# Kernel optimization log

Hardware: AMD Instinct MI355X
Metric: run time of the kernel (lower is better)

## Reference

```python
import jax, jax.numpy as jnp
import numpy as np

N_NODES = 200_000
N_EDGES = 6_400_000
EMB = 32      # emb_hidden_dim
HID = 16      # hidden_dim
BY = 4        # num_birthyear_disc
NSYMP = 15    # num_symp (rm_feature=-999)
NOPT = 3      # replace_missing_value='replace'


def setup_inputs() -> dict:
    key = jax.random.key(0)
    ks = jax.random.split(key, 12)
    # node features: [one-hot birth (4) | gender (1) | 15 symptom codes]
    birth_cat = jax.random.randint(ks[0], (N_NODES,), 0, BY)
    birth_oh = jax.nn.one_hot(birth_cat, BY, dtype=jnp.int32)
    gender = jax.random.randint(ks[1], (N_NODES, 1), 0, 2, dtype=jnp.int32)
    symp = jax.random.randint(ks[2], (N_NODES, NSYMP), 0, NOPT, dtype=jnp.int32)
    x = jnp.concatenate([birth_oh, gender, symp], axis=1)  # [N, 20] int32
    edge_index = jax.random.randint(ks[3], (2, N_EDGES), 0, N_NODES, dtype=jnp.int64)
    s = 0.1
    return {
        "x": x,
        "edge_index": edge_index,
        "birth_table": jax.random.normal(ks[4], (BY, EMB), jnp.float32) * s,
        "gender_table": jax.random.normal(ks[5], (2, EMB), jnp.float32) * s,
        "symp_tables": jax.random.normal(ks[6], (NSYMP, NOPT, EMB), jnp.float32) * s,
        "W1": jax.random.normal(ks[7], (EMB, HID), jnp.float32) * s,
        "b1": jnp.zeros((HID,), jnp.float32),
        "W2": jax.random.normal(ks[8], (HID, HID), jnp.float32) * s,
        "b2": jnp.zeros((HID,), jnp.float32),
        "Wl": jax.random.normal(ks[9], (HID, 1), jnp.float32) * s,
        "bl": jnp.zeros((1,), jnp.float32),
    }


def _gcn_conv(h, W, b, src, tgt, n):
    # PyG GCNConv: linear (no bias) -> symmetric normalization w/ self-loops -> scatter-add -> +bias
    h = h @ W                                    # [N, out]
    msg = h[src] * None if False else h[src]     # gather source features
    deg = jax.ops.segment_sum(jnp.ones_like(tgt, dtype=h.dtype), tgt, num_segments=n)
    dinv = jnp.where(deg > 0, jax.lax.rsqrt(jnp.maximum(deg, 1e-12)), 0.0)
    norm = dinv[src] * dinv[tgt]                 # [E+N]
    out = jax.ops.segment_sum(norm[:, None] * msg, tgt, num_segments=n)
    return out + b


def reference(x, edge_index, birth_table, gender_table, symp_tables, W1, b1, W2, b2, Wl, bl):
    n = x.shape[0]
    birth_idx = jnp.argmax(x[:, :BY], axis=1)                 # column of the 1 in one-hot
    birth_embs = birth_table[birth_idx]                       # [N, EMB]
    gender_embs = gender_table[x[:, BY].astype(jnp.int32)]    # [N, EMB]
    symp_idx = x[:, -NSYMP:].astype(jnp.int32)                # [N, 15]
    feat_embs = jnp.mean(symp_tables[jnp.arange(NSYMP)[None, :], symp_idx], axis=1)  # [N, EMB]
    h = (birth_embs + gender_embs + feat_embs) / 3.0          # mean of the three stacks
    # dropout is identity in eval mode
    # self-loops added once (identical for both convs)
    loop = jnp.arange(n, dtype=edge_index.dtype)
    src = jnp.concatenate([edge_index[0], loop])
    tgt = jnp.concatenate([edge_index[1], loop])
    h = jax.nn.elu(_gcn_conv(h, W1, b1, src, tgt, n))
    h = _gcn_conv(h, W2, b2, src, tgt, n)
    return h @ Wl + bl                                        # [N, 1]
```

## Files before the change

kernel.cpp:

```cpp
#include <hip/hip_runtime.h>
#include <hip/hip_fp16.h>
#include <math.h>

#define EMB 32
#define HID 16
#define BY 4
#define NSYMP 15
#define NOPT 3
#define XCOLS (BY + 1 + NSYMP)

#define BSHIFT 8
#define BSZ 256
#define EPB 4096
#define NBCAP 1024
#define SPT 4
#define LSTCAP 10240

#define SCAN_T 256
#define SCAN_E 32
#define SCAN_B (SCAN_T * SCAN_E)

__device__ __forceinline__ unsigned int wave_incl_scan(unsigned int v, int lane) {
#pragma unroll
    for (int off = 1; off < 64; off <<= 1) {
        unsigned int u = __shfl_up(v, off, 64);
        if (lane >= off) v += u;
    }
    return v;
}

__global__ __launch_bounds__(256) void k_hist(const int* __restrict__ tgt,
                                              unsigned int* __restrict__ H,
                                              int nE, int gb1, int nbins) {
    __shared__ unsigned int h[NBCAP];
    int b = blockIdx.x, tid = threadIdx.x;
    for (int k = tid; k < NBCAP; k += 256) h[k] = 0;
    __syncthreads();
    int e0 = b * EPB;
    int ecnt = min(EPB, nE - e0);
    for (int k = tid; k < ecnt; k += 256)
        atomicAdd(&h[(unsigned)tgt[e0 + k] >> BSHIFT], 1u);
    __syncthreads();
    for (int q = tid; q < nbins; q += 256) H[(size_t)q * gb1 + b] = h[q];
}

__global__ __launch_bounds__(256) void k_bsum(const unsigned int* __restrict__ A,
                                              unsigned int* __restrict__ bsum, int m) {
    __shared__ unsigned int s[SCAN_T];
    int base = blockIdx.x * SCAN_B + threadIdx.x * SCAN_E;
    unsigned int t = 0;
#pragma unroll
    for (int k = 0; k < SCAN_E; ++k) { int idx = base + k; if (idx < m) t += A[idx]; }
    s[threadIdx.x] = t; __syncthreads();
    for (int off = SCAN_T / 2; off > 0; off >>= 1) {
        if (threadIdx.x < off) s[threadIdx.x] += s[threadIdx.x + off];
        __syncthreads();
    }
    if (threadIdx.x == 0) bsum[blockIdx.x] = s[0];
}

__global__ __launch_bounds__(512) void k_bscan(const unsigned int* __restrict__ bsum,
                                               unsigned int* __restrict__ boff, int nb) {
    __shared__ unsigned int s[512];
    unsigned int v = (threadIdx.x < (unsigned)nb) ? bsum[threadIdx.x] : 0u;
    s[threadIdx.x] = v; __syncthreads();
    for (int off = 1; off < 512; off <<= 1) {
        unsigned int t = (threadIdx.x >= (unsigned)off) ? s[threadIdx.x - off] : 0u;
        __syncthreads();
        s[threadIdx.x] += t;
        __syncthreads();
    }
    if (threadIdx.x < (unsigned)nb) boff[threadIdx.x] = s[threadIdx.x] - v;
}

__global__ __launch_bounds__(256) void k_scan2(const unsigned int* __restrict__ A,
                                               const unsigned int* __restrict__ boff,
                                               unsigned int* __restrict__ S, int m, int total) {
    __shared__ unsigned int s[SCAN_T];
    int tid = threadIdx.x;
    int base = blockIdx.x * SCAN_B + tid * SCAN_E;
    unsigned int t = 0;
#pragma unroll
    for (int k = 0; k < SCAN_E; ++k) { int idx = base + k; if (idx < m) t += A[idx]; }
    s[tid] = t; __syncthreads();
    unsigned int own = t;
    for (int off = 1; off < SCAN_T; off <<= 1) {
        unsigned int u = (tid >= off) ? s[tid - off] : 0u;
        __syncthreads();
        s[tid] += u;
        __syncthreads();
    }
    unsigned int run = boff[blockIdx.x] + s[tid] - own;
#pragma unroll
    for (int k = 0; k < SCAN_E; ++k) {
        int idx = base + k;
        if (idx < m) { S[idx] = run; run += A[idx]; }
    }
    if (blockIdx.x == 0 && tid == 0) S[m] = (unsigned int)total;
}

__global__ __launch_bounds__(256) void k_scat(const int* __restrict__ tgt,
                                              const int* __restrict__ src,
                                              const unsigned int* __restrict__ S,
                                              int* __restrict__ bp,
                                              int nE, int gb1, int nbins) {
    __shared__ int bpv[EPB];
    __shared__ unsigned short qid[EPB];
    __shared__ unsigned int cur[NBCAP];
    __shared__ unsigned int dif[NBCAP];
    __shared__ unsigned int wsum[4];
    int b = blockIdx.x, tid = threadIdx.x;
    int lane = tid & 63, wid = tid >> 6;
    for (int k = tid; k < NBCAP; k += 256) cur[k] = 0;
    __syncthreads();
    int e0 = b * EPB;
    int ecnt = min(EPB, nE - e0);

    for (int k = tid; k < ecnt; k += 256)
        atomicAdd(&cur[(unsigned)tgt[e0 + k] >> BSHIFT], 1u);
    __syncthreads();

    unsigned int lv[SPT]; unsigned int tsum = 0;
#pragma unroll
    for (int k = 0; k < SPT; ++k) {
        int f = SPT * tid + k;
        lv[k] = tsum; tsum += cur[f];
    }
    unsigned int incl = wave_incl_scan(tsum, lane);
    if (lane == 63) wsum[wid] = incl;
    __syncthreads();
    unsigned int woff = 0;
    for (int w = 0; w < wid; ++w) woff += wsum[w];
    unsigned int excl = woff + incl - tsum;
    __syncthreads();
#pragma unroll
    for (int k = 0; k < SPT; ++k) {
        int f = SPT * tid + k;
        cur[f] = excl + lv[k]; dif[f] = excl + lv[k];
    }
    __syncthreads();
    for (int q = tid; q < nbins; q += 256)
        dif[q] = S[(size_t)q * gb1 + b] - dif[q];
    __syncthreads();

    for (int k = tid; k < ecnt; k += 256) {
        int t = tgt[e0 + k];
        int q = (unsigned)t >> BSHIFT;
        unsigned int lpos = atomicAdd(&cur[q], 1u);
        bpv[lpos] = (src[e0 + k] << BSHIFT) | (t & (BSZ - 1));
        qid[lpos] = (unsigned short)q;
    }
    __syncthreads();

    for (int k = tid; k < ecnt; k += 256) {
        int q = qid[k];
        bp[dif[q] + k] = bpv[k];
    }
}

__global__ __launch_bounds__(256) void k_bcsr(const unsigned int* __restrict__ S,
                                              const int* __restrict__ bp,
                                              unsigned int* __restrict__ rowptr,
                                              int* __restrict__ col,
                                              float* __restrict__ dinv,
                                              int n, int gb1) {
    __shared__ int lst[LSTCAP];
    __shared__ unsigned int h[BSZ];
    __shared__ unsigned int cu[BSZ];
    __shared__ unsigned int wsum[4];
    int q = blockIdx.x, tid = threadIdx.x;
    int lane = tid & 63, wid = tid >> 6;
    h[tid] = 0;
    __syncthreads();
    unsigned int e0 = S[(size_t)q * gb1];
    unsigned int e1 = S[(size_t)(q + 1) * gb1];
    int cnt = (int)(e1 - e0);
    for (int k = tid; k < cnt; k += 256)
        atomicAdd(&h[bp[e0 + k] & (BSZ - 1)], 1u);
    __syncthreads();
    unsigned int own = h[tid];
    unsigned int incl = wave_incl_scan(own, lane);
    if (lane == 63) wsum[wid] = incl;
    __syncthreads();
    unsigned int woff = 0;
    for (int w = 0; w < wid; ++w) woff += wsum[w];
    unsigned int excl = woff + incl - own;
    cu[tid] = excl;
    int i = (q << BSHIFT) + tid;
    if (i <= n) rowptr[i] = e0 + excl;
    if (i < n) {
        float d = (float)(own + 1u);
        float r = rsqrtf(d);
        r = r * (1.5f - 0.5f * d * r * r);
        dinv[i] = r;
    }
    __syncthreads();
    for (int k = tid; k < cnt; k += 256) {
        int v = bp[e0 + k];
        unsigned int pos = atomicAdd(&cu[v & (BSZ - 1)], 1u);
        lst[pos] = (unsigned)v >> BSHIFT;
    }
    __syncthreads();
    for (int k = tid; k < cnt; k += 256)
        col[e0 + k] = lst[k];
}

__global__ __launch_bounds__(256) void k_embed(const int* __restrict__ x,
                                               const float* __restrict__ birth_t,
                                               const float* __restrict__ gender_t,
                                               const float* __restrict__ symp_t,
                                               const float* __restrict__ W1,
                                               const float* __restrict__ dinv,
                                               __half* __restrict__ A16, int n) {
    __shared__ float sB[BY * EMB];
    __shared__ float sG[2 * EMB];
    __shared__ float sS[NSYMP * NOPT * EMB];
    __shared__ float sW[EMB * HID];
    for (int k = threadIdx.x; k < BY * EMB; k += blockDim.x) sB[k] = birth_t[k];
    for (int k = threadIdx.x; k < 2 * EMB; k += blockDim.x) sG[k] = gender_t[k];
    for (int k = threadIdx.x; k < NSYMP * NOPT * EMB; k += blockDim.x) sS[k] = symp_t[k];
    for (int k = threadIdx.x; k < EMB * HID; k += blockDim.x) sW[k] = W1[k];
    __syncthreads();

    int i = blockIdx.x * blockDim.x + threadIdx.x;
    if (i >= n) return;

    const int* xr = x + (size_t)i * XCOLS;
    int xv[XCOLS];
#pragma unroll
    for (int k = 0; k < XCOLS; ++k) xv[k] = xr[k];

    int bi = 0;
#pragma unroll
    for (int k = 1; k < BY; ++k) if (xv[k] > xv[bi]) bi = k;
    int gi = xv[BY];

    float ssum[EMB];
#pragma unroll
    for (int k = 0; k < EMB; ++k) ssum[k] = 0.f;
#pragma unroll
    for (int j = 0; j < NSYMP; ++j) {
        const float* row = &sS[(j * NOPT + xv[BY + 1 + j]) * EMB];
#pragma unroll
        for (int k = 0; k < EMB; ++k) ssum[k] += row[k];
    }

    float h[EMB];
#pragma unroll
    for (int k = 0; k < EMB; ++k)
        h[k] = (sB[bi * EMB + k] + sG[gi * EMB + k] + ssum[k] * (1.f / 15.f)) * (1.f / 3.f);

    float hp[HID];
#pragma unroll
    for (int j = 0; j < HID; ++j) hp[j] = 0.f;
#pragma unroll
    for (int k = 0; k < EMB; ++k) {
        float hv = h[k];
#pragma unroll
        for (int j = 0; j < HID; ++j) hp[j] += hv * sW[k * HID + j];
    }

    float dv = dinv[i];
    __half2 t2[8];
#pragma unroll
    for (int j = 0; j < 8; ++j)
        t2[j] = __floats2half2_rn(dv * hp[2 * j], dv * hp[2 * j + 1]);
    uint4* o = (uint4*)(A16 + (size_t)i * HID);
    o[0] = *(uint4*)&t2[0];
    o[1] = *(uint4*)&t2[4];
}

__global__ __launch_bounds__(256) void k_gmid5(const unsigned int* __restrict__ rowptr,
                                               const int* __restrict__ col,
                                               const __half* __restrict__ A16,
                                               const float* __restrict__ dinv,
                                               const float* __restrict__ W2,
                                               const float* __restrict__ b1,
                                               const float* __restrict__ Wl,
                                               float* __restrict__ z, int n) {
    __shared__ float sW[HID * HID];
    __shared__ float sb[HID];
    __shared__ float sw[HID];
    __shared__ float sAcc[16][HID];
    if (threadIdx.x < HID * HID) sW[threadIdx.x] = W2[threadIdx.x];
    if (threadIdx.x < HID) { sb[threadIdx.x] = b1[threadIdx.x]; sw[threadIdx.x] = Wl[threadIdx.x]; }
    __syncthreads();

    int gg = threadIdx.x >> 4;
    int l  = threadIdx.x & 15;
    int p  = l >> 1;
    int hc = l & 1;
    int i = blockIdx.x * 16 + gg;
    bool valid = (i < n);

    unsigned int r0 = 0, r1 = 0;
    if (valid) { r0 = rowptr[i]; r1 = rowptr[i + 1]; }

    float a[8];
#pragma unroll
    for (int k = 0; k < 8; ++k) a[k] = 0.f;

    unsigned int e = r0;
    for (; e + 16 <= r1; e += 16) {
        int s0 = col[e + p];
        int s1 = col[e + 8 + p];
        uint4 raw0 = *((const uint4*)(A16 + (size_t)s0 * HID) + hc);
        uint4 raw1 = *((const uint4*)(A16 + (size_t)s1 * HID) + hc);
        const __half2* h0 = (const __half2*)&raw0;
        const __half2* h1 = (const __half2*)&raw1;
#pragma unroll
        for (int k = 0; k < 4; ++k) {
            float2 f0 = __half22float2(h0[k]);
            float2 f1 = __half22float2(h1[k]);
            a[2 * k]     += f0.x + f1.x;
            a[2 * k + 1] += f0.y + f1.y;
        }
    }
    for (; e + 8 <= r1; e += 8) {
        int s0 = col[e + p];
        uint4 raw0 = *((const uint4*)(A16 + (size_t)s0 * HID) + hc);
        const __half2* h0 = (const __half2*)&raw0;
#pragma unroll
        for (int k = 0; k < 4; ++k) {
            float2 f0 = __half22float2(h0[k]);
            a[2 * k]     += f0.x;
            a[2 * k + 1] += f0.y;
        }
    }
    if (e + p < r1) {
        int s0 = col[e + p];
        uint4 raw0 = *((const uint4*)(A16 + (size_t)s0 * HID) + hc);
        const __half2* h0 = (const __half2*)&raw0;
#pragma unroll
        for (int k = 0; k < 4; ++k) {
            float2 f0 = __half22float2(h0[k]);
            a[2 * k]     += f0.x;
            a[2 * k + 1] += f0.y;
        }
    }
#pragma unroll
    for (int k = 0; k < 8; ++k) {
        a[k] += __shfl_xor(a[k], 2, 64);
        a[k] += __shfl_xor(a[k], 4, 64);
        a[k] += __shfl_xor(a[k], 8, 64);
    }
    if (l < 2) {
        float4* d0 = (float4*)&sAcc[gg][hc * 8];
        d0[0] = make_float4(a[0], a[1], a[2], a[3]);
        d0[1] = make_float4(a[4], a[5], a[6], a[7]);
    }
    __syncthreads();

    float dv = valid ? dinv[i] : 0.f;
    float self = valid ? __half2float(A16[(size_t)i * HID + l]) : 0.f;
    float v = dv * (sAcc[gg][l] + self) + sb[l];
    float h1 = (v > 0.f) ? v : expm1f(v);

    int lanebase = (threadIdx.x & 63) & ~15;
    float hp = 0.f;
#pragma unroll
    for (int k = 0; k < HID; ++k)
        hp += __shfl(h1, lanebase + k, 64) * sW[k * HID + l];
    float pz = dv * hp * sw[l];
#pragma unroll
    for (int off = 8; off > 0; off >>= 1) pz += __shfl_xor(pz, off, 64);
    if (l == 0 && valid) z[i] = pz;
}

__global__ __launch_bounds__(256) void k_gfin4(const unsigned int* __restrict__ rowptr,
                                               const int* __restrict__ col,
                                               const float* __restrict__ z,
                                               const float* __restrict__ dinv,
                                               const float* __restrict__ b2,
                                               const float* __restrict__ Wl,
                                               const float* __restrict__ bl,
                                               float* __restrict__ out, int n) {
    __shared__ float sc0;
    if (threadIdx.x == 0) {
        float c = 0.f;
#pragma unroll
        for (int k = 0; k < HID; ++k) c += b2[k] * Wl[k];
        sc0 = c + bl[0];
    }
    __syncthreads();

    int i = blockIdx.x * blockDim.x + threadIdx.x;
    if (i >= n) return;

    unsigned int r0 = rowptr[i];
    unsigned int r1 = rowptr[i + 1];
    float s0 = 0.f, s1 = 0.f, s2 = 0.f, s3 = 0.f;
    float s4 = 0.f, s5 = 0.f, s6 = 0.f, s7 = 0.f;
    unsigned int e = r0;
    for (; e + 8 <= r1; e += 8) {
        s0 += z[col[e + 0]]; s1 += z[col[e + 1]];
        s2 += z[col[e + 2]]; s3 += z[col[e + 3]];
        s4 += z[col[e + 4]]; s5 += z[col[e + 5]];
        s6 += z[col[e + 6]]; s7 += z[col[e + 7]];
    }
    for (; e < r1; ++e) s0 += z[col[e]];
    float s = ((s0 + s1) + (s2 + s3)) + ((s4 + s5) + (s6 + s7));
    out[i] = dinv[i] * (s + z[i]) + sc0;
}

extern "C" void kernel_launch(void* const* d_in, const int* in_sizes, int n_in,
                              void* d_out, int out_size, void* d_ws, size_t ws_size,
                              hipStream_t stream) {
    const int*   x        = (const int*)d_in[0];
    const int*   ei       = (const int*)d_in[1];
    const float* birth_t  = (const float*)d_in[2];
    const float* gender_t = (const float*)d_in[3];
    const float* symp_t   = (const float*)d_in[4];
    const float* W1       = (const float*)d_in[5];
    const float* b1       = (const float*)d_in[6];
    const float* W2       = (const float*)d_in[7];
    const float* b2       = (const float*)d_in[8];
    const float* Wl       = (const float*)d_in[9];
    const float* bl       = (const float*)d_in[10];
    float*       out      = (float*)d_out;

    const int n  = in_sizes[0] / XCOLS;
    const int nE = in_sizes[1] / 2;
    const int* src = ei;
    const int* tgt = ei + nE;

    const int nbuck = (n + BSZ - 1) >> BSHIFT;
    const int gb1   = (nE + EPB - 1) / EPB;
    const int M     = nbuck * gb1;
    const int nb    = (M + SCAN_B - 1) / SCAN_B;

    char* ws = (char*)d_ws;
    size_t off = 0;
    auto alloc = [&](size_t bytes) { char* p = ws + off; off = (off + bytes + 255) & ~(size_t)255; return p; };
    unsigned int* H      = (unsigned int*)alloc((size_t)M * 4);
    unsigned int* S      = (unsigned int*)alloc(((size_t)M + 1) * 4);
    unsigned int* bsum   = (unsigned int*)alloc(512 * 4);
    unsigned int* boff   = (unsigned int*)alloc(512 * 4);
    int*          bp     = (int*)alloc((size_t)nE * 4);
    int*          col    = (int*)alloc((size_t)nE * 4);
    unsigned int* rowptr = (unsigned int*)alloc(((size_t)n + 1) * 4);
    float*        dinv   = (float*)alloc((size_t)n * 4);
    __half*       A16    = (__half*)alloc((size_t)n * HID * 2);
    float*        z      = (float*)alloc((size_t)n * 4);

    const int BLK = 256;
    const int gN    = (n + BLK - 1) / BLK;
    const int gNode = (n + 15) / 16;

    k_hist <<<gb1, BLK, 0, stream>>>(tgt, H, nE, gb1, nbuck);
    k_bsum <<<nb, SCAN_T, 0, stream>>>(H, bsum, M);
    k_bscan<<<1, 512, 0, stream>>>(bsum, boff, nb);
    k_scan2<<<nb, SCAN_T, 0, stream>>>(H, boff, S, M, nE);
    k_scat <<<gb1, BLK, 0, stream>>>(tgt, src, S, bp, nE, gb1, nbuck);
    k_bcsr <<<nbuck, BLK, 0, stream>>>(S, bp, rowptr, col, dinv, n, gb1);
    k_embed<<<gN, BLK, 0, stream>>>(x, birth_t, gender_t, symp_t, W1, dinv, A16, n);
    k_gmid5<<<gNode, BLK, 0, stream>>>(rowptr, col, A16, dinv, W2, b1, Wl, z, n);
    k_gfin4<<<gN, BLK, 0, stream>>>(rowptr, col, z, dinv, b2, Wl, bl, out, n);
}
```

Before: 258.9 us.

## Use fixed 512 blocks for bucket scatter and write edges directly to global

The edge histogram and scatter now run on a fixed grid of 512 blocks with about 12.5k edges each, down from 1563 blocks of 4096 edges. That shrinks the histogram and scan matrix. The scatter kernel no longer re-counts, scans and stages edges in shared memory; it seeds per-bucket cursors from the global scan and writes each packed edge straight to its global slot through a shared atomic. This removes a shared-memory pass and several barriers, but the global writes become scattered, and fewer blocks may reduce parallelism.

```diff
diff --git a/kernel.cpp b/kernel.cpp
--- a/kernel.cpp
+++ b/kernel.cpp
@@ -11,9 +11,8 @@
 
 #define BSHIFT 8
 #define BSZ 256
-#define EPB 4096
+#define NBLK 512
 #define NBCAP 1024
-#define SPT 4
 #define LSTCAP 10240
 
 #define SCAN_T 256
@@ -31,17 +30,17 @@
 
 __global__ __launch_bounds__(256) void k_hist(const int* __restrict__ tgt,
                                               unsigned int* __restrict__ H,
-                                              int nE, int gb1, int nbins) {
+                                              int nE, int epb, int nbuck) {
     __shared__ unsigned int h[NBCAP];
     int b = blockIdx.x, tid = threadIdx.x;
     for (int k = tid; k < NBCAP; k += 256) h[k] = 0;
     __syncthreads();
-    int e0 = b * EPB;
-    int ecnt = min(EPB, nE - e0);
+    int e0 = b * epb;
+    int ecnt = min(epb, nE - e0);
     for (int k = tid; k < ecnt; k += 256)
         atomicAdd(&h[(unsigned)tgt[e0 + k] >> BSHIFT], 1u);
     __syncthreads();
-    for (int q = tid; q < nbins; q += 256) H[(size_t)q * gb1 + b] = h[q];
+    for (int q = tid; q < nbuck; q += 256) H[(size_t)q * NBLK + b] = h[q];
 }
 
 __global__ __launch_bounds__(256) void k_bsum(const unsigned int* __restrict__ A,
@@ -103,58 +102,19 @@
                                               const int* __restrict__ src,
                                               const unsigned int* __restrict__ S,
                                               int* __restrict__ bp,
-                                              int nE, int gb1, int nbins) {
-    __shared__ int bpv[EPB];
-    __shared__ unsigned short qid[EPB];
+                                              int nE, int epb, int nbuck) {
     __shared__ unsigned int cur[NBCAP];
-    __shared__ unsigned int dif[NBCAP];
-    __shared__ unsigned int wsum[4];
     int b = blockIdx.x, tid = threadIdx.x;
-    int lane = tid & 63, wid = tid >> 6;
-    for (int k = tid; k < NBCAP; k += 256) cur[k] = 0;
-    __syncthreads();
-    int e0 = b * EPB;
-    int ecnt = min(EPB, nE - e0);
-
-    for (int k = tid; k < ecnt; k += 256)
-        atomicAdd(&cur[(unsigned)tgt[e0 + k] >> BSHIFT], 1u);
-    __syncthreads();
-
-    unsigned int lv[SPT]; unsigned int tsum = 0;
-#pragma unroll
-    for (int k = 0; k < SPT; ++k) {
-        int f = SPT * tid + k;
-        lv[k] = tsum; tsum += cur[f];
-    }
-    unsigned int incl = wave_incl_scan(tsum, lane);
-    if (lane == 63) wsum[wid] = incl;
-    __syncthreads();
-    unsigned int woff = 0;
-    for (int w = 0; w < wid; ++w) woff += wsum[w];
-    unsigned int excl = woff + incl - tsum;
-    __syncthreads();
-#pragma unroll
-    for (int k = 0; k < SPT; ++k) {
-        int f = SPT * tid + k;
-        cur[f] = excl + lv[k]; dif[f] = excl + lv[k];
-    }
-    __syncthreads();
-    for (int q = tid; q < nbins; q += 256)
-        dif[q] = S[(size_t)q * gb1 + b] - dif[q];
-    __syncthreads();
-
+    for (int q = tid; q < nbuck; q += 256) cur[q] = S[(size_t)q * NBLK + b];
+    __syncthreads();
+    int e0 = b * epb;
+    int ecnt = min(epb, nE - e0);
     for (int k = tid; k < ecnt; k += 256) {
         int t = tgt[e0 + k];
+        int s = src[e0 + k];
         int q = (unsigned)t >> BSHIFT;
-        unsigned int lpos = atomicAdd(&cur[q], 1u);
-        bpv[lpos] = (src[e0 + k] << BSHIFT) | (t & (BSZ - 1));
-        qid[lpos] = (unsigned short)q;
-    }
-    __syncthreads();
-
-    for (int k = tid; k < ecnt; k += 256) {
-        int q = qid[k];
-        bp[dif[q] + k] = bpv[k];
+        unsigned int pos = atomicAdd(&cur[q], 1u);
+        bp[pos] = (s << BSHIFT) | (t & (BSZ - 1));
     }
 }
 
@@ -163,7 +123,7 @@
                                               unsigned int* __restrict__ rowptr,
                                               int* __restrict__ col,
                                               float* __restrict__ dinv,
-                                              int n, int gb1) {
+                                              int n) {
     __shared__ int lst[LSTCAP];
     __shared__ unsigned int h[BSZ];
     __shared__ unsigned int cu[BSZ];
@@ -172,8 +132,8 @@
     int lane = tid & 63, wid = tid >> 6;
     h[tid] = 0;
     __syncthreads();
-    unsigned int e0 = S[(size_t)q * gb1];
-    unsigned int e1 = S[(size_t)(q + 1) * gb1];
+    unsigned int e0 = S[(size_t)q * NBLK];
+    unsigned int e1 = S[(size_t)(q + 1) * NBLK];
     int cnt = (int)(e1 - e0);
     for (int k = tid; k < cnt; k += 256)
         atomicAdd(&h[bp[e0 + k] & (BSZ - 1)], 1u);
@@ -425,8 +385,8 @@
     const int* tgt = ei + nE;
 
     const int nbuck = (n + BSZ - 1) >> BSHIFT;
-    const int gb1   = (nE + EPB - 1) / EPB;
-    const int M     = nbuck * gb1;
+    const int epb   = (nE + NBLK - 1) / NBLK;
+    const int M     = nbuck * NBLK;
     const int nb    = (M + SCAN_B - 1) / SCAN_B;
 
     char* ws = (char*)d_ws;
@@ -447,12 +407,12 @@
     const int gN    = (n + BLK - 1) / BLK;
     const int gNode = (n + 15) / 16;
 
-    k_hist <<<gb1, BLK, 0, stream>>>(tgt, H, nE, gb1, nbuck);
+    k_hist <<<NBLK, BLK, 0, stream>>>(tgt, H, nE, epb, nbuck);
     k_bsum <<<nb, SCAN_T, 0, stream>>>(H, bsum, M);
     k_bscan<<<1, 512, 0, stream>>>(bsum, boff, nb);
     k_scan2<<<nb, SCAN_T, 0, stream>>>(H, boff, S, M, nE);
-    k_scat <<<gb1, BLK, 0, stream>>>(tgt, src, S, bp, nE, gb1, nbuck);
-    k_bcsr <<<nbuck, BLK, 0, stream>>>(S, bp, rowptr, col, dinv, n, gb1);
+    k_scat <<<NBLK, BLK, 0, stream>>>(tgt, src, S, bp, nE, epb, nbuck);
+    k_bcsr <<<nbuck, BLK, 0, stream>>>(S, bp, rowptr, col, dinv, n);
     k_embed<<<gN, BLK, 0, stream>>>(x, birth_t, gender_t, symp_t, W1, dinv, A16, n);
     k_gmid5<<<gNode, BLK, 0, stream>>>(rowptr, col, A16, dinv, W2, b1, Wl, z, n);
     k_gfin4<<<gN, BLK, 0, stream>>>(rowptr, col, z, dinv, b2, Wl, bl, out, n);
```

Measured after the change: 274.9 us. 6.2% more time.

## Drop histogram and global scan passes by storing per-block bucket segments

Applied to the files above, without the earlier changes.

The separate histogram kernel and three-kernel global scan are removed. Instead, each scatter block writes its edges bucket-sorted into its own contiguous slot and records its per-bucket local offsets. A small per-bucket reduction then computes global bucket starts, and the CSR kernel gathers each bucket's segments from every block into shared memory before the per-row sort. This removes an extra read of the target array, several kernel launches and the large offset matrix scan. In exchange the CSR kernel does many short serial per-thread copies from scattered locations and writes col directly with scattered stores. The edges-per-block count is also doubled.

```diff
diff --git a/kernel.cpp b/kernel.cpp
--- a/kernel.cpp
+++ b/kernel.cpp
@@ -11,14 +11,11 @@
 
 #define BSHIFT 8
 #define BSZ 256
-#define EPB 4096
+#define EPB 8192
 #define NBCAP 1024
 #define SPT 4
+#define SPT2 4
 #define LSTCAP 10240
-
-#define SCAN_T 256
-#define SCAN_E 32
-#define SCAN_B (SCAN_T * SCAN_E)
 
 __device__ __forceinline__ unsigned int wave_incl_scan(unsigned int v, int lane) {
 #pragma unroll
@@ -29,85 +26,13 @@
     return v;
 }
 
-__global__ __launch_bounds__(256) void k_hist(const int* __restrict__ tgt,
-                                              unsigned int* __restrict__ H,
-                                              int nE, int gb1, int nbins) {
-    __shared__ unsigned int h[NBCAP];
-    int b = blockIdx.x, tid = threadIdx.x;
-    for (int k = tid; k < NBCAP; k += 256) h[k] = 0;
-    __syncthreads();
-    int e0 = b * EPB;
-    int ecnt = min(EPB, nE - e0);
-    for (int k = tid; k < ecnt; k += 256)
-        atomicAdd(&h[(unsigned)tgt[e0 + k] >> BSHIFT], 1u);
-    __syncthreads();
-    for (int q = tid; q < nbins; q += 256) H[(size_t)q * gb1 + b] = h[q];
-}
-
-__global__ __launch_bounds__(256) void k_bsum(const unsigned int* __restrict__ A,
-                                              unsigned int* __restrict__ bsum, int m) {
-    __shared__ unsigned int s[SCAN_T];
-    int base = blockIdx.x * SCAN_B + threadIdx.x * SCAN_E;
-    unsigned int t = 0;
-#pragma unroll
-    for (int k = 0; k < SCAN_E; ++k) { int idx = base + k; if (idx < m) t += A[idx]; }
-    s[threadIdx.x] = t; __syncthreads();
-    for (int off = SCAN_T / 2; off > 0; off >>= 1) {
-        if (threadIdx.x < off) s[threadIdx.x] += s[threadIdx.x + off];
-        __syncthreads();
-    }
-    if (threadIdx.x == 0) bsum[blockIdx.x] = s[0];
-}
-
-__global__ __launch_bounds__(512) void k_bscan(const unsigned int* __restrict__ bsum,
-                                               unsigned int* __restrict__ boff, int nb) {
-    __shared__ unsigned int s[512];
-    unsigned int v = (threadIdx.x < (unsigned)nb) ? bsum[threadIdx.x] : 0u;
-    s[threadIdx.x] = v; __syncthreads();
-    for (int off = 1; off < 512; off <<= 1) {
-        unsigned int t = (threadIdx.x >= (unsigned)off) ? s[threadIdx.x - off] : 0u;
-        __syncthreads();
-        s[threadIdx.x] += t;
-        __syncthreads();
-    }
-    if (threadIdx.x < (unsigned)nb) boff[threadIdx.x] = s[threadIdx.x] - v;
-}
-
-__global__ __launch_bounds__(256) void k_scan2(const unsigned int* __restrict__ A,
-                                               const unsigned int* __restrict__ boff,
-                                               unsigned int* __restrict__ S, int m, int total) {
-    __shared__ unsigned int s[SCAN_T];
-    int tid = threadIdx.x;
-    int base = blockIdx.x * SCAN_B + tid * SCAN_E;
-    unsigned int t = 0;
-#pragma unroll
-    for (int k = 0; k < SCAN_E; ++k) { int idx = base + k; if (idx < m) t += A[idx]; }
-    s[tid] = t; __syncthreads();
-    unsigned int own = t;
-    for (int off = 1; off < SCAN_T; off <<= 1) {
-        unsigned int u = (tid >= off) ? s[tid - off] : 0u;
-        __syncthreads();
-        s[tid] += u;
-        __syncthreads();
-    }
-    unsigned int run = boff[blockIdx.x] + s[tid] - own;
-#pragma unroll
-    for (int k = 0; k < SCAN_E; ++k) {
-        int idx = base + k;
-        if (idx < m) { S[idx] = run; run += A[idx]; }
-    }
-    if (blockIdx.x == 0 && tid == 0) S[m] = (unsigned int)total;
-}
-
 __global__ __launch_bounds__(256) void k_scat(const int* __restrict__ tgt,
                                               const int* __restrict__ src,
-                                              const unsigned int* __restrict__ S,
+                                              unsigned int* __restrict__ L,
                                               int* __restrict__ bp,
-                                              int nE, int gb1, int nbins) {
+                                              int nE, int gb1, int nbuck) {
     __shared__ int bpv[EPB];
-    __shared__ unsigned short qid[EPB];
     __shared__ unsigned int cur[NBCAP];
-    __shared__ unsigned int dif[NBCAP];
     __shared__ unsigned int wsum[4];
     int b = blockIdx.x, tid = threadIdx.x;
     int lane = tid & 63, wid = tid >> 6;
@@ -136,11 +61,10 @@
 #pragma unroll
     for (int k = 0; k < SPT; ++k) {
         int f = SPT * tid + k;
-        cur[f] = excl + lv[k]; dif[f] = excl + lv[k];
-    }
-    __syncthreads();
-    for (int q = tid; q < nbins; q += 256)
-        dif[q] = S[(size_t)q * gb1 + b] - dif[q];
+        unsigned int v = excl + lv[k];
+        cur[f] = v;
+        if (f <= nbuck) L[(size_t)f * gb1 + b] = v;
+    }
     __syncthreads();
 
     for (int k = tid; k < ecnt; k += 256) {
@@ -148,17 +72,29 @@
         int q = (unsigned)t >> BSHIFT;
         unsigned int lpos = atomicAdd(&cur[q], 1u);
         bpv[lpos] = (src[e0 + k] << BSHIFT) | (t & (BSZ - 1));
-        qid[lpos] = (unsigned short)q;
-    }
-    __syncthreads();
-
-    for (int k = tid; k < ecnt; k += 256) {
-        int q = qid[k];
-        bp[dif[q] + k] = bpv[k];
-    }
-}
-
-__global__ __launch_bounds__(256) void k_bcsr(const unsigned int* __restrict__ S,
+    }
+    __syncthreads();
+
+    for (int k = tid; k < ecnt; k += 256)
+        bp[e0 + k] = bpv[k];
+}
+
+__global__ __launch_bounds__(256) void k_rsum(const unsigned int* __restrict__ L,
+                                              unsigned int* __restrict__ R, int gb1) {
+    __shared__ unsigned int s[256];
+    int q = blockIdx.x, tid = threadIdx.x;
+    unsigned int t = 0;
+    for (int b = tid; b < gb1; b += 256) t += L[(size_t)q * gb1 + b];
+    s[tid] = t; __syncthreads();
+    for (int off = 128; off > 0; off >>= 1) {
+        if (tid < off) s[tid] += s[tid + off];
+        __syncthreads();
+    }
+    if (tid == 0) R[q] = s[0];
+}
+
+__global__ __launch_bounds__(256) void k_bcsr(const unsigned int* __restrict__ L,
+                                              const unsigned int* __restrict__ R,
                                               const int* __restrict__ bp,
                                               unsigned int* __restrict__ rowptr,
                                               int* __restrict__ col,
@@ -170,24 +106,52 @@
     __shared__ unsigned int wsum[4];
     int q = blockIdx.x, tid = threadIdx.x;
     int lane = tid & 63, wid = tid >> 6;
-    h[tid] = 0;
-    __syncthreads();
-    unsigned int e0 = S[(size_t)q * gb1];
-    unsigned int e1 = S[(size_t)(q + 1) * gb1];
-    int cnt = (int)(e1 - e0);
-    for (int k = tid; k < cnt; k += 256)
-        atomicAdd(&h[bp[e0 + k] & (BSZ - 1)], 1u);
-    __syncthreads();
-    unsigned int own = h[tid];
-    unsigned int incl = wave_incl_scan(own, lane);
+    const unsigned int* Lq0 = L + (size_t)q * gb1;
+    const unsigned int* Lq1 = L + (size_t)(q + 1) * gb1;
+
+    unsigned int st_[SPT2], ln_[SPT2], lvb[SPT2];
+    unsigned int tsum = 0;
+#pragma unroll
+    for (int k = 0; k < SPT2; ++k) {
+        int b = tid * SPT2 + k;
+        unsigned int st = 0, ln = 0;
+        if (b < gb1) { st = Lq0[b]; ln = Lq1[b] - st; }
+        st_[k] = st; ln_[k] = ln; lvb[k] = tsum; tsum += ln;
+    }
+    unsigned int incl = wave_incl_scan(tsum, lane);
     if (lane == 63) wsum[wid] = incl;
     __syncthreads();
     unsigned int woff = 0;
     for (int w = 0; w < wid; ++w) woff += wsum[w];
-    unsigned int excl = woff + incl - own;
+    unsigned int base = woff + incl - tsum;
+#pragma unroll
+    for (int k = 0; k < SPT2; ++k) {
+        int b = tid * SPT2 + k;
+        if (b < gb1 && ln_[k]) {
+            const int* sp = bp + (size_t)b * EPB + st_[k];
+            unsigned int pos = base + lvb[k];
+            for (unsigned int j = 0; j < ln_[k]; ++j) lst[pos + j] = sp[j];
+        }
+    }
+    h[tid] = 0;
+    __syncthreads();
+
+    unsigned int r0g = R[q];
+    int cnt = (int)(R[q + 1] - r0g);
+
+    for (int k = tid; k < cnt; k += 256)
+        atomicAdd(&h[lst[k] & (BSZ - 1)], 1u);
+    __syncthreads();
+    unsigned int own = h[tid];
+    unsigned int incl2 = wave_incl_scan(own, lane);
+    if (lane == 63) wsum[wid] = incl2;
+    __syncthreads();
+    unsigned int woff2 = 0;
+    for (int w = 0; w < wid; ++w) woff2 += wsum[w];
+    unsigned int excl = woff2 + incl2 - own;
     cu[tid] = excl;
     int i = (q << BSHIFT) + tid;
-    if (i <= n) rowptr[i] = e0 + excl;
+    if (i <= n) rowptr[i] = r0g + excl;
     if (i < n) {
         float d = (float)(own + 1u);
         float r = rsqrtf(d);
@@ -195,14 +159,12 @@
         dinv[i] = r;
     }
     __syncthreads();
+
     for (int k = tid; k < cnt; k += 256) {
-        int v = bp[e0 + k];
+        int v = lst[k];
         unsigned int pos = atomicAdd(&cu[v & (BSZ - 1)], 1u);
-        lst[pos] = (unsigned)v >> BSHIFT;
-    }
-    __syncthreads();
-    for (int k = tid; k < cnt; k += 256)
-        col[e0 + k] = lst[k];
+        col[r0g + pos] = (unsigned)v >> BSHIFT;
+    }
 }
 
 __global__ __launch_bounds__(256) void k_embed(const int* __restrict__ x,
@@ -426,17 +388,13 @@
 
     const int nbuck = (n + BSZ - 1) >> BSHIFT;
     const int gb1   = (nE + EPB - 1) / EPB;
-    const int M     = nbuck * gb1;
-    const int nb    = (M + SCAN_B - 1) / SCAN_B;
 
     char* ws = (char*)d_ws;
     size_t off = 0;
     auto alloc = [&](size_t bytes) { char* p = ws + off; off = (off + bytes + 255) & ~(size_t)255; return p; };
-    unsigned int* H      = (unsigned int*)alloc((size_t)M * 4);
-    unsigned int* S      = (unsigned int*)alloc(((size_t)M + 1) * 4);
-    unsigned int* bsum   = (unsigned int*)alloc(512 * 4);
-    unsigned int* boff   = (unsigned int*)alloc(512 * 4);
-    int*          bp     = (int*)alloc((size_t)nE * 4);
+    unsigned int* L      = (unsigned int*)alloc((size_t)(nbuck + 1) * gb1 * 4);
+    unsigned int* R      = (unsigned int*)alloc((size_t)(nbuck + 1) * 4);
+    int*          bp     = (int*)alloc((size_t)gb1 * EPB * 4);
     int*          col    = (int*)alloc((size_t)nE * 4);
     unsigned int* rowptr = (unsigned int*)alloc(((size_t)n + 1) * 4);
     float*        dinv   = (float*)alloc((size_t)n * 4);
@@ -447,12 +405,9 @@
     const int gN    = (n + BLK - 1) / BLK;
     const int gNode = (n + 15) / 16;
 
-    k_hist <<<gb1, BLK, 0, stream>>>(tgt, H, nE, gb1, nbuck);
-    k_bsum <<<nb, SCAN_T, 0, stream>>>(H, bsum, M);
-    k_bscan<<<1, 512, 0, stream>>>(bsum, boff, nb);
-    k_scan2<<<nb, SCAN_T, 0, stream>>>(H, boff, S, M, nE);
-    k_scat <<<gb1, BLK, 0, stream>>>(tgt, src, S, bp, nE, gb1, nbuck);
-    k_bcsr <<<nbuck, BLK, 0, stream>>>(S, bp, rowptr, col, dinv, n, gb1);
+    k_scat <<<gb1, BLK, 0, stream>>>(tgt, src, L, bp, nE, gb1, nbuck);
+    k_rsum <<<nbuck + 1, BLK, 0, stream>>>(L, R, gb1);
+    k_bcsr <<<nbuck, BLK, 0, stream>>>(L, R, bp, rowptr, col, dinv, n, gb1);
     k_embed<<<gN, BLK, 0, stream>>>(x, birth_t, gender_t, symp_t, W1, dinv, A16, n);
     k_gmid5<<<gNode, BLK, 0, stream>>>(rowptr, col, A16, dinv, W2, b1, Wl, z, n);
     k_gfin4<<<gN, BLK, 0, stream>>>(rowptr, col, z, dinv, b2, Wl, bl, out, n);
```

New measurement: 239.6 us. -7.4%, faster.
